# Kernel tuning notes

Hardware: AMD Instinct MI355X
Metric: run time of the kernel (lower is better)

Reference implementation:

```python
import jax, jax.numpy as jnp
import numpy as np

B, S, D, H = 4, 2048, 2048, 16
DH = D // H


def setup_inputs() -> dict:
    key = jax.random.key(0)
    ks = jax.random.split(key, 11)
    p = 0.02  # keep pre-softmax logits in a sane range
    return {
        "x": jax.random.normal(ks[0], (B, S, D), jnp.float32),
        "Wq": jax.random.normal(ks[1], (D, D), jnp.float32) * p,
        "bq": jax.random.normal(ks[2], (D,), jnp.float32) * p,
        "Wk": jax.random.normal(ks[3], (D, D), jnp.float32) * p,
        "bk": jax.random.normal(ks[4], (D,), jnp.float32) * p,
        "Wv": jax.random.normal(ks[5], (D, D), jnp.float32) * p,
        "bv": jax.random.normal(ks[6], (D,), jnp.float32) * p,
        "Wo": jax.random.normal(ks[7], (D, D), jnp.float32) * p,
        "bo": jax.random.normal(ks[8], (D,), jnp.float32) * p,
        "spiral_weight": jax.random.normal(ks[9], (H,), jnp.float32),
        "helix_rotation": jax.random.normal(ks[10], (D,), jnp.float32),
    }


def reference(x, Wq, bq, Wk, bk, Wv, bv, Wo, bo, spiral_weight, helix_rotation):
    b, s, d = x.shape
    h, dh = H, d // H
    # projections (torch Linear: x @ W.T + b), split into heads
    q = (x @ Wq.T + bq).reshape(b, s, h, dh)
    k = (x @ Wk.T + bk).reshape(b, s, h, dh)
    v = (x @ Wv.T + bv).reshape(b, s, h, dh)
    # cos/sin helix gating, applied per (head, head_dim) channel
    rot = helix_rotation.reshape(h, dh)
    q = q * jnp.cos(rot)
    k = k * jnp.sin(rot)
    # per-head scaled scores: [b,h,s,s]
    scores = jnp.einsum("bshd,bthd->bhst", q, k) / np.sqrt(dh).astype(np.float32)
    scores = scores * spiral_weight[None, :, None, None]
    attn = jax.nn.softmax(scores, axis=-1)
    out = jnp.einsum("bhst,bthd->bshd", attn, v).reshape(b, s, d)
    return out @ Wo.T + bo
```

## Files before the change

kernel.cpp:

```cpp
#include <hip/hip_runtime.h>
#include <math.h>

#define B_ 4
#define S_ 2048
#define D_ 2048
#define H_ 16
#define DH_ 128

typedef unsigned short u16;
typedef unsigned int u32;
typedef u16 u16x8 __attribute__((ext_vector_type(8)));
typedef __bf16 bf16x8 __attribute__((ext_vector_type(8)));
typedef float f32x4 __attribute__((ext_vector_type(4)));

__device__ inline u16 f2bf(float f) {
    unsigned int u = __builtin_bit_cast(unsigned int, f);
    unsigned int lsb = (u >> 16) & 1u;
    u += 0x7fffu + lsb;
    return (u16)(u >> 16);
}

__device__ inline f32x4 mfma16(u16x8 a, u16x8 b, f32x4 c) {
    return __builtin_amdgcn_mfma_f32_16x16x32_bf16(
        __builtin_bit_cast(bf16x8, a), __builtin_bit_cast(bf16x8, b), c, 0, 0, 0);
}

__device__ inline void gl2lds16(const u16* g, u16* l) {
    __builtin_amdgcn_global_load_lds(
        (const __attribute__((address_space(1))) void*)g,
        (__attribute__((address_space(3))) void*)l, 16, 0, 0);
}

__global__ __launch_bounds__(256) void cvt_f32_bf16(const float* __restrict__ src,
                                                    u16* __restrict__ dst, int n8) {
    int i = blockIdx.x * 256 + threadIdx.x;
    if (i >= n8) return;
    const float4* s = (const float4*)src + (size_t)i * 2;
    float4 a = s[0], b = s[1];
    u16x8 o;
    o[0] = f2bf(a.x); o[1] = f2bf(a.y); o[2] = f2bf(a.z); o[3] = f2bf(a.w);
    o[4] = f2bf(b.x); o[5] = f2bf(b.y); o[6] = f2bf(b.z); o[7] = f2bf(b.w);
    *((u16x8*)dst + i) = o;
}

template <int GATE, int TRANSV, typename OutT>
__global__ __launch_bounds__(256) void gemm_bt(const u16* __restrict__ A,
                                               const u16* __restrict__ Bw,
                                               const float* __restrict__ bias,
                                               const float* __restrict__ helix,
                                               OutT* __restrict__ C,
                                               int M, int N, int K) {
    __shared__ __align__(16) u16 As[128 * 64];
    __shared__ __align__(16) u16 Bs[128 * 64];

    const int tid = threadIdx.x;
    const int lane = tid & 63, w = tid >> 6;
    const int lr = lane & 15, quad = lane >> 4;
    const int wm = w & 1, wn = w >> 1;
    const int tm = blockIdx.y, tn = blockIdx.x;

    const u16* Ab = A + (size_t)(tm * 128) * K;
    const u16* Bb = Bw + (size_t)(tn * 128) * K;

    const u16* gA[4];
    const u16* gB[4];
    u16* lA[4];
    u16* lB[4];
#pragma unroll
    for (int q = 0; q < 4; ++q) {
        int seg = w * 4 + q;
        int row = seg * 8 + (lane >> 3);
        int gcol = ((lane & 7) ^ (row & 7)) * 8;
        gA[q] = Ab + (size_t)row * K + gcol;
        gB[q] = Bb + (size_t)row * K + gcol;
        lA[q] = As + seg * 512;
        lB[q] = Bs + seg * 512;
    }

    f32x4 zero = {0.f, 0.f, 0.f, 0.f};
    f32x4 acc[4][4];
#pragma unroll
    for (int im = 0; im < 4; ++im)
#pragma unroll
        for (int jn = 0; jn < 4; ++jn) acc[im][jn] = zero;

    const int rA = wm * 64 + lr;
    const int rB = wn * 64 + lr;
    const int sw = lr & 7;

    for (int kt = 0; kt < K; kt += 64) {
        __syncthreads();
#pragma unroll
        for (int q = 0; q < 4; ++q) gl2lds16(gA[q] + kt, lA[q]);
#pragma unroll
        for (int q = 0; q < 4; ++q) gl2lds16(gB[q] + kt, lB[q]);
        __syncthreads();

#pragma unroll
        for (int s = 0; s < 2; ++s) {
            const int kc = ((s * 4 + quad) ^ sw) * 8;
            u16x8 af[4], bf[4];
#pragma unroll
            for (int im = 0; im < 4; ++im)
                af[im] = *(const u16x8*)&As[(rA + im * 16) * 64 + kc];
#pragma unroll
            for (int jn = 0; jn < 4; ++jn)
                bf[jn] = *(const u16x8*)&Bs[(rB + jn * 16) * 64 + kc];
#pragma unroll
            for (int im = 0; im < 4; ++im)
#pragma unroll
                for (int jn = 0; jn < 4; ++jn)
                    acc[im][jn] = mfma16(af[im], bf[jn], acc[im][jn]);
        }
    }

    if constexpr (TRANSV) {
        __shared__ __align__(16) u16 Ts[128 * 72];
        const int grow = tm * 128;
        const int bb = grow / S_;
        const int t0g = grow % S_;
#pragma unroll
        for (int hb = 0; hb < 2; ++hb) {
            __syncthreads();
            if (wm == hb) {
#pragma unroll
                for (int jn = 0; jn < 4; ++jn) {
                    float bs = bias[tn * 128 + wn * 64 + jn * 16 + lr];
#pragma unroll
                    for (int im = 0; im < 4; ++im)
#pragma unroll
                        for (int r = 0; r < 4; ++r)
                            Ts[(wn * 64 + jn * 16 + lr) * 72 + im * 16 + quad * 4 + r] =
                                f2bf(acc[im][jn][r] + bs);
                }
            }
            __syncthreads();
#pragma unroll
            for (int p = 0; p < 4; ++p) {
                int idx = p * 256 + tid;
                int dh_l = idx & 127, tb8 = idx >> 7;
                u16x8 o = *(const u16x8*)&Ts[dh_l * 72 + tb8 * 8];
                int gd = tn * 128 + dh_l;
                int hh = gd >> 7, dhm = gd & 127;
                u16* dst = (u16*)C + (((size_t)bb * H_ + hh) * DH_ + dhm) * S_ + t0g +
                           hb * 64 + tb8 * 8;
                *(u16x8*)dst = o;
            }
        }
    } else {
#pragma unroll
        for (int jn = 0; jn < 4; ++jn) {
            int col = tn * 128 + wn * 64 + jn * 16 + lr;
            float bs = bias[col];
            float g = 1.0f;
            if (GATE == 1) g = cosf(helix[col]);
            if (GATE == 2) g = sinf(helix[col]);
#pragma unroll
            for (int im = 0; im < 4; ++im)
#pragma unroll
                for (int r = 0; r < 4; ++r) {
                    int row = tm * 128 + wm * 64 + im * 16 + quad * 4 + r;
                    float val = (acc[im][jn][r] + bs) * g;
                    if constexpr (sizeof(OutT) == 2)
                        ((u16*)C)[(size_t)row * N + col] = f2bf(val);
                    else
                        ((float*)C)[(size_t)row * N + col] = val;
                }
        }
    }
}

__global__ __launch_bounds__(256, 2) void helix_attn(const u16* __restrict__ Q,
                                                     const u16* __restrict__ Kq,
                                                     const u16* __restrict__ Vt,
                                                     const float* __restrict__ spiral,
                                                     u16* __restrict__ O) {
    __shared__ __align__(16) u16 Ks[64 * 136];
    __shared__ __align__(16) u16 Vs[128 * 72];
    __shared__ __align__(16) u16 Ps[128 * 80];

    const int tid = threadIdx.x;
    const int lane = tid & 63, w = tid >> 6;
    const int lr = lane & 15, quad = lane >> 4;

    const int bx = blockIdx.x;
    const int qt = bx & 15;
    const int h = (bx >> 4) & 15;
    const int b = bx >> 8;

    const size_t headoff = (size_t)b * S_ * D_ + (size_t)h * DH_;
    const u16* qp = Q + headoff;
    const u16* kp = Kq + headoff;
    const u16* vtp = Vt + ((size_t)b * H_ + h) * (size_t)DH_ * S_;

    const float scale2 = spiral[h] * 0.08838834764831845f * 1.4426950408889634f;

    u16x8 qf[2][4];
#pragma unroll
    for (int mb = 0; mb < 2; ++mb)
#pragma unroll
        for (int c = 0; c < 4; ++c) {
            u16x8 raw = *(const u16x8*)(qp + (size_t)(qt * 128 + mb * 64 + w * 16 + lr) * D_ +
                                        c * 32 + quad * 8);
#pragma unroll
            for (int j = 0; j < 8; ++j) {
                float f = __builtin_bit_cast(float, (u32)raw[j] << 16) * scale2;
                qf[mb][c][j] = f2bf(f);
            }
        }

    f32x4 zero = {0.f, 0.f, 0.f, 0.f};
    f32x4 Oacc[2][8];
#pragma unroll
    for (int mb = 0; mb < 2; ++mb)
#pragma unroll
        for (int n = 0; n < 8; ++n) Oacc[mb][n] = zero;
    float rs[2][4] = {{0.f, 0.f, 0.f, 0.f}, {0.f, 0.f, 0.f, 0.f}};

    for (int tt = 0; tt < 32; ++tt) {
        const int t0 = tt * 64;
        __syncthreads();
#pragma unroll
        for (int p = 0; p < 4; ++p) {
            int lin = p * 256 + tid;
            int trow = lin >> 4;
            int ch = (lin & 15) * 8;
            *(u16x8*)&Ks[trow * 136 + ch] =
                *(const u16x8*)(kp + (size_t)(t0 + trow) * D_ + ch);
            int drow = lin >> 3;
            int tch = (lin & 7) * 8;
            *(u16x8*)&Vs[drow * 72 + tch] =
                *(const u16x8*)(vtp + (size_t)drow * S_ + t0 + tch);
        }
        __syncthreads();

        f32x4 Sacc[2][4] = {{zero, zero, zero, zero}, {zero, zero, zero, zero}};
#pragma unroll
        for (int c = 0; c < 4; ++c) {
#pragma unroll
            for (int j = 0; j < 4; ++j) {
                u16x8 kf = *(const u16x8*)&Ks[(j * 16 + lr) * 136 + c * 32 + quad * 8];
                Sacc[0][j] = mfma16(qf[0][c], kf, Sacc[0][j]);
                Sacc[1][j] = mfma16(qf[1][c], kf, Sacc[1][j]);
            }
        }

#pragma unroll
        for (int mb = 0; mb < 2; ++mb)
#pragma unroll
            for (int j = 0; j < 4; ++j)
#pragma unroll
                for (int r = 0; r < 4; ++r) {
                    float p = exp2f(Sacc[mb][j][r]);
                    u32 u = __builtin_bit_cast(u32, p);
                    rs[mb][r] += __builtin_bit_cast(float, u & 0xffff0000u);
                    Ps[(mb * 64 + w * 16 + quad * 4 + r) * 80 + j * 16 + lr] = (u16)(u >> 16);
                }

#pragma unroll
        for (int ks = 0; ks < 2; ++ks) {
            u16x8 pf0 = *(const u16x8*)&Ps[(w * 16 + lr) * 80 + ks * 32 + quad * 8];
            u16x8 pf1 = *(const u16x8*)&Ps[(64 + w * 16 + lr) * 80 + ks * 32 + quad * 8];
#pragma unroll
            for (int n = 0; n < 8; ++n) {
                u16x8 vf = *(const u16x8*)&Vs[(n * 16 + lr) * 72 + ks * 32 + quad * 8];
                Oacc[0][n] = mfma16(pf0, vf, Oacc[0][n]);
                Oacc[1][n] = mfma16(pf1, vf, Oacc[1][n]);
            }
        }
    }

#pragma unroll
    for (int mb = 0; mb < 2; ++mb)
#pragma unroll
        for (int r = 0; r < 4; ++r) {
            float s = rs[mb][r];
#pragma unroll
            for (int off = 1; off < 16; off <<= 1) s += __shfl_xor(s, off, 64);
            float inv = 1.0f / s;
            int row = qt * 128 + mb * 64 + w * 16 + quad * 4 + r;
            u16* op = O + headoff + (size_t)row * D_;
#pragma unroll
            for (int n = 0; n < 8; ++n) op[n * 16 + lr] = f2bf(Oacc[mb][n][r] * inv);
        }
}

extern "C" void kernel_launch(void* const* d_in, const int* in_sizes, int n_in,
                              void* d_out, int out_size, void* d_ws, size_t ws_size,
                              hipStream_t stream) {
    const float* x = (const float*)d_in[0];
    const float* Wq = (const float*)d_in[1];
    const float* bq = (const float*)d_in[2];
    const float* Wk = (const float*)d_in[3];
    const float* bk = (const float*)d_in[4];
    const float* Wv = (const float*)d_in[5];
    const float* bv = (const float*)d_in[6];
    const float* Wo = (const float*)d_in[7];
    const float* bo = (const float*)d_in[8];
    const float* spiral = (const float*)d_in[9];
    const float* helix = (const float*)d_in[10];
    float* out = (float*)d_out;

    char* ws = (char*)d_ws;
    u16* xbf = (u16*)(ws);
    u16* wqb = (u16*)(ws + 33554432);
    u16* wkb = (u16*)(ws + 33554432 + 8388608);
    u16* wvb = (u16*)(ws + 33554432 + 16777216);
    u16* wob = (u16*)(ws + 33554432 + 25165824);
    u16* qb = (u16*)(ws + 67108864);
    u16* kb = (u16*)(ws + 67108864 + 33554432);
    u16* vtb = (u16*)(ws + 67108864 + 67108864);
    u16* attnb = xbf;

    const int ND = D_ * D_;
    const int NX = B_ * S_ * D_;

    cvt_f32_bf16<<<NX / 8 / 256, 256, 0, stream>>>(x, xbf, NX / 8);
    cvt_f32_bf16<<<ND / 8 / 256, 256, 0, stream>>>(Wq, wqb, ND / 8);
    cvt_f32_bf16<<<ND / 8 / 256, 256, 0, stream>>>(Wk, wkb, ND / 8);
    cvt_f32_bf16<<<ND / 8 / 256, 256, 0, stream>>>(Wv, wvb, ND / 8);
    cvt_f32_bf16<<<ND / 8 / 256, 256, 0, stream>>>(Wo, wob, ND / 8);

    dim3 gg(D_ / 128, (B_ * S_) / 128);
    gemm_bt<1, 0, u16><<<gg, 256, 0, stream>>>(xbf, wqb, bq, helix, qb, B_ * S_, D_, D_);
    gemm_bt<2, 0, u16><<<gg, 256, 0, stream>>>(xbf, wkb, bk, helix, kb, B_ * S_, D_, D_);
    gemm_bt<0, 1, u16><<<gg, 256, 0, stream>>>(xbf, wvb, bv, nullptr, vtb, B_ * S_, D_, D_);

    helix_attn<<<B_ * H_ * (S_ / 128), 256, 0, stream>>>(qb, kb, vtb, spiral, attnb);

    gemm_bt<0, 0, float><<<gg, 256, 0, stream>>>(attnb, wob, bo, nullptr, out, B_ * S_, D_, D_);
}
```

Measured before the change: 697.4 us.

## Replace projection GEMMs with 256x256 double-buffered, ping-pong scheduled kernel

Replaces the 128x128 single-buffered GEMM with a 256x256-tile, 512-thread kernel. It double-buffers LDS and splits each k-step into four MFMA quarter phases, issuing the next tile's global-to-LDS loads between them and raising wave priority during MFMA bursts. The V projection is recomputed as Wv·xᵀ, so the output comes out already transposed per head without the LDS transpose epilogue. This aims to hide load latency and raise arithmetic intensity. The costs are a larger LDS footprint (128KB per block), more barriers, and scalar strided stores in the V epilogue.

```diff
diff --git a/kernel.cpp b/kernel.cpp
--- a/kernel.cpp
+++ b/kernel.cpp
@@ -29,6 +29,12 @@
     __builtin_amdgcn_global_load_lds(
         (const __attribute__((address_space(1))) void*)g,
         (__attribute__((address_space(3))) void*)l, 16, 0, 0);
+}
+
+__device__ inline void block_barrier() {
+    asm volatile("" ::: "memory");
+    __builtin_amdgcn_s_barrier();
+    asm volatile("" ::: "memory");
 }
 
 __global__ __launch_bounds__(256) void cvt_f32_bf16(const float* __restrict__ src,
@@ -43,123 +49,188 @@
     *((u16x8*)dst + i) = o;
 }
 
-template <int GATE, int TRANSV, typename OutT>
-__global__ __launch_bounds__(256) void gemm_bt(const u16* __restrict__ A,
-                                               const u16* __restrict__ Bw,
-                                               const float* __restrict__ bias,
-                                               const float* __restrict__ helix,
-                                               OutT* __restrict__ C,
-                                               int M, int N, int K) {
-    __shared__ __align__(16) u16 As[128 * 64];
-    __shared__ __align__(16) u16 Bs[128 * 64];
+template <int GATE, int VOUT, typename OutT>
+__global__ __launch_bounds__(512, 2) void gemm256(const u16* __restrict__ A,
+                                                  const u16* __restrict__ Bw,
+                                                  const float* __restrict__ bias,
+                                                  const float* __restrict__ helix,
+                                                  OutT* __restrict__ C,
+                                                  int M, int N, int K) {
+    __shared__ __align__(16) u16 As[2][256 * 64];
+    __shared__ __align__(16) u16 Bs[2][256 * 64];
 
     const int tid = threadIdx.x;
     const int lane = tid & 63, w = tid >> 6;
     const int lr = lane & 15, quad = lane >> 4;
     const int wm = w & 1, wn = w >> 1;
     const int tm = blockIdx.y, tn = blockIdx.x;
-
-    const u16* Ab = A + (size_t)(tm * 128) * K;
-    const u16* Bb = Bw + (size_t)(tn * 128) * K;
-
-    const u16* gA[4];
-    const u16* gB[4];
-    u16* lA[4];
-    u16* lB[4];
-#pragma unroll
-    for (int q = 0; q < 4; ++q) {
-        int seg = w * 4 + q;
-        int row = seg * 8 + (lane >> 3);
-        int gcol = ((lane & 7) ^ (row & 7)) * 8;
-        gA[q] = Ab + (size_t)row * K + gcol;
-        gB[q] = Bb + (size_t)row * K + gcol;
-        lA[q] = As + seg * 512;
-        lB[q] = Bs + seg * 512;
+    const int NT = K >> 6;
+
+    const u16* Asrc = A + (size_t)(tm * 256) * K;
+    const u16* Bsrc = Bw + (size_t)(tn * 256) * K;
+
+    u32 go[4][2];
+    u32 lo[4][2];
+#pragma unroll
+    for (int q = 0; q < 2; ++q) {
+        const int seg = w * 2 + q;
+        const int i0 = seg * 8 + (lane >> 3);
+        const int s0 = seg * 8;
+        int row = (i0 & 63) | ((i0 >> 6) << 7);
+        int rb = (s0 & 63) | ((s0 >> 6) << 7);
+        go[0][q] = (u32)row * K + (((lane & 7) ^ (row & 7)) << 3);
+        lo[0][q] = rb << 6;
+        row += 64; rb += 64;
+        go[3][q] = (u32)row * K + (((lane & 7) ^ (row & 7)) << 3);
+        lo[3][q] = rb << 6;
+        row = (i0 & 31) | ((i0 >> 5) << 6);
+        rb = (s0 & 31) | ((s0 >> 5) << 6);
+        go[1][q] = (u32)row * K + (((lane & 7) ^ (row & 7)) << 3);
+        lo[1][q] = rb << 6;
+        row += 32; rb += 32;
+        go[2][q] = (u32)row * K + (((lane & 7) ^ (row & 7)) << 3);
+        lo[2][q] = rb << 6;
     }
 
+#define STAGE(u, tt)                                                          \
+    do {                                                                      \
+        const int kt_ = (((tt) < NT) ? (tt) : (NT - 1)) << 6;                 \
+        const u16* gb_ = ((u) == 1 || (u) == 2) ? Bsrc : Asrc;                \
+        u16* lb_ = ((u) == 1 || (u) == 2) ? Bs[(tt) & 1] : As[(tt) & 1];      \
+        gl2lds16(gb_ + go[u][0] + kt_, lb_ + lo[u][0]);                       \
+        gl2lds16(gb_ + go[u][1] + kt_, lb_ + lo[u][1]);                       \
+    } while (0)
+
+    const int koff0 = (quad * 8) ^ ((lr & 7) * 8);
+    const int koff1 = (32 + quad * 8) ^ ((lr & 7) * 8);
+    const int rA = wm * 128 + lr;
+    const int rB = wn * 64 + lr;
+
     f32x4 zero = {0.f, 0.f, 0.f, 0.f};
-    f32x4 acc[4][4];
-#pragma unroll
-    for (int im = 0; im < 4; ++im)
+    f32x4 acc[8][4];
+#pragma unroll
+    for (int im = 0; im < 8; ++im)
 #pragma unroll
         for (int jn = 0; jn < 4; ++jn) acc[im][jn] = zero;
 
-    const int rA = wm * 64 + lr;
-    const int rB = wn * 64 + lr;
-    const int sw = lr & 7;
-
-    for (int kt = 0; kt < K; kt += 64) {
-        __syncthreads();
-#pragma unroll
-        for (int q = 0; q < 4; ++q) gl2lds16(gA[q] + kt, lA[q]);
-#pragma unroll
-        for (int q = 0; q < 4; ++q) gl2lds16(gB[q] + kt, lB[q]);
-        __syncthreads();
-
-#pragma unroll
-        for (int s = 0; s < 2; ++s) {
-            const int kc = ((s * 4 + quad) ^ sw) * 8;
-            u16x8 af[4], bf[4];
+    u16x8 af[4][2], bf[4][2];
+
+    STAGE(0, 0); STAGE(1, 0); STAGE(2, 0); STAGE(3, 0);
+    STAGE(0, 1); STAGE(1, 1); STAGE(2, 1);
+    asm volatile("s_waitcnt vmcnt(6)" ::: "memory");
+    block_barrier();
+
+    for (int t = 0; t < NT; ++t) {
+        const u16* Ab = As[t & 1];
+        const u16* Bb = Bs[t & 1];
+
+#pragma unroll
+        for (int im = 0; im < 4; ++im) {
+            af[im][0] = *(const u16x8*)&Ab[(rA + im * 16) * 64 + koff0];
+            af[im][1] = *(const u16x8*)&Ab[(rA + im * 16) * 64 + koff1];
+        }
+#pragma unroll
+        for (int jn = 0; jn < 2; ++jn) {
+            bf[jn][0] = *(const u16x8*)&Bb[(rB + jn * 16) * 64 + koff0];
+            bf[jn][1] = *(const u16x8*)&Bb[(rB + jn * 16) * 64 + koff1];
+        }
+        STAGE(3, t + 1);
+        block_barrier();
+        asm volatile("s_waitcnt lgkmcnt(0)" ::: "memory");
+        __builtin_amdgcn_s_setprio(1);
+#pragma unroll
+        for (int s = 0; s < 2; ++s)
 #pragma unroll
             for (int im = 0; im < 4; ++im)
-                af[im] = *(const u16x8*)&As[(rA + im * 16) * 64 + kc];
-#pragma unroll
-            for (int jn = 0; jn < 4; ++jn)
-                bf[jn] = *(const u16x8*)&Bs[(rB + jn * 16) * 64 + kc];
+#pragma unroll
+                for (int jn = 0; jn < 2; ++jn)
+                    acc[im][jn] = mfma16(af[im][s], bf[jn][s], acc[im][jn]);
+        __builtin_amdgcn_s_setprio(0);
+        block_barrier();
+
+#pragma unroll
+        for (int jn = 2; jn < 4; ++jn) {
+            bf[jn][0] = *(const u16x8*)&Bb[(rB + jn * 16) * 64 + koff0];
+            bf[jn][1] = *(const u16x8*)&Bb[(rB + jn * 16) * 64 + koff1];
+        }
+        STAGE(0, t + 2);
+        block_barrier();
+        asm volatile("s_waitcnt lgkmcnt(0)" ::: "memory");
+        __builtin_amdgcn_s_setprio(1);
+#pragma unroll
+        for (int s = 0; s < 2; ++s)
 #pragma unroll
             for (int im = 0; im < 4; ++im)
 #pragma unroll
-                for (int jn = 0; jn < 4; ++jn)
-                    acc[im][jn] = mfma16(af[im], bf[jn], acc[im][jn]);
-        }
+                for (int jn = 2; jn < 4; ++jn)
+                    acc[im][jn] = mfma16(af[im][s], bf[jn][s], acc[im][jn]);
+        __builtin_amdgcn_s_setprio(0);
+        block_barrier();
+
+#pragma unroll
+        for (int im = 0; im < 4; ++im) {
+            af[im][0] = *(const u16x8*)&Ab[(rA + 64 + im * 16) * 64 + koff0];
+            af[im][1] = *(const u16x8*)&Ab[(rA + 64 + im * 16) * 64 + koff1];
+        }
+        STAGE(1, t + 2);
+        block_barrier();
+        asm volatile("s_waitcnt lgkmcnt(0)" ::: "memory");
+        __builtin_amdgcn_s_setprio(1);
+#pragma unroll
+        for (int s = 0; s < 2; ++s)
+#pragma unroll
+            for (int im = 0; im < 4; ++im)
+#pragma unroll
+                for (int jn = 0; jn < 2; ++jn)
+                    acc[im + 4][jn] = mfma16(af[im][s], bf[jn][s], acc[im + 4][jn]);
+        __builtin_amdgcn_s_setprio(0);
+        block_barrier();
+
+        STAGE(2, t + 2);
+        asm volatile("s_waitcnt vmcnt(6)" ::: "memory");
+        block_barrier();
+        __builtin_amdgcn_s_setprio(1);
+#pragma unroll
+        for (int s = 0; s < 2; ++s)
+#pragma unroll
+            for (int im = 0; im < 4; ++im)
+#pragma unroll
+                for (int jn = 2; jn < 4; ++jn)
+                    acc[im + 4][jn] = mfma16(af[im][s], bf[jn][s], acc[im + 4][jn]);
+        __builtin_amdgcn_s_setprio(0);
+        block_barrier();
     }
-
-    if constexpr (TRANSV) {
-        __shared__ __align__(16) u16 Ts[128 * 72];
-        const int grow = tm * 128;
-        const int bb = grow / S_;
-        const int t0g = grow % S_;
-#pragma unroll
-        for (int hb = 0; hb < 2; ++hb) {
-            __syncthreads();
-            if (wm == hb) {
+    asm volatile("s_waitcnt vmcnt(0)" ::: "memory");
+#undef STAGE
+
+    if constexpr (VOUT) {
+#pragma unroll
+        for (int im = 0; im < 8; ++im)
+#pragma unroll
+            for (int r = 0; r < 4; ++r) {
+                int row = tm * 256 + wm * 128 + im * 16 + quad * 4 + r;
+                float bs = bias[row];
 #pragma unroll
                 for (int jn = 0; jn < 4; ++jn) {
-                    float bs = bias[tn * 128 + wn * 64 + jn * 16 + lr];
-#pragma unroll
-                    for (int im = 0; im < 4; ++im)
-#pragma unroll
-                        for (int r = 0; r < 4; ++r)
-                            Ts[(wn * 64 + jn * 16 + lr) * 72 + im * 16 + quad * 4 + r] =
-                                f2bf(acc[im][jn][r] + bs);
+                    int col = tn * 256 + wn * 64 + jn * 16 + lr;
+                    float val = acc[im][jn][r] + bs;
+                    ((u16*)C)[(size_t)(col >> 11) * ((size_t)D_ * S_) +
+                              (size_t)row * S_ + (col & (S_ - 1))] = f2bf(val);
                 }
             }
-            __syncthreads();
-#pragma unroll
-            for (int p = 0; p < 4; ++p) {
-                int idx = p * 256 + tid;
-                int dh_l = idx & 127, tb8 = idx >> 7;
-                u16x8 o = *(const u16x8*)&Ts[dh_l * 72 + tb8 * 8];
-                int gd = tn * 128 + dh_l;
-                int hh = gd >> 7, dhm = gd & 127;
-                u16* dst = (u16*)C + (((size_t)bb * H_ + hh) * DH_ + dhm) * S_ + t0g +
-                           hb * 64 + tb8 * 8;
-                *(u16x8*)dst = o;
-            }
-        }
     } else {
 #pragma unroll
         for (int jn = 0; jn < 4; ++jn) {
-            int col = tn * 128 + wn * 64 + jn * 16 + lr;
+            int col = tn * 256 + wn * 64 + jn * 16 + lr;
             float bs = bias[col];
             float g = 1.0f;
             if (GATE == 1) g = cosf(helix[col]);
             if (GATE == 2) g = sinf(helix[col]);
 #pragma unroll
-            for (int im = 0; im < 4; ++im)
+            for (int im = 0; im < 8; ++im)
 #pragma unroll
                 for (int r = 0; r < 4; ++r) {
-                    int row = tm * 128 + wm * 64 + im * 16 + quad * 4 + r;
+                    int row = tm * 256 + wm * 128 + im * 16 + quad * 4 + r;
                     float val = (acc[im][jn][r] + bs) * g;
                     if constexpr (sizeof(OutT) == 2)
                         ((u16*)C)[(size_t)row * N + col] = f2bf(val);
@@ -321,12 +392,13 @@
     cvt_f32_bf16<<<ND / 8 / 256, 256, 0, stream>>>(Wv, wvb, ND / 8);
     cvt_f32_bf16<<<ND / 8 / 256, 256, 0, stream>>>(Wo, wob, ND / 8);
 
-    dim3 gg(D_ / 128, (B_ * S_) / 128);
-    gemm_bt<1, 0, u16><<<gg, 256, 0, stream>>>(xbf, wqb, bq, helix, qb, B_ * S_, D_, D_);
-    gemm_bt<2, 0, u16><<<gg, 256, 0, stream>>>(xbf, wkb, bk, helix, kb, B_ * S_, D_, D_);
-    gemm_bt<0, 1, u16><<<gg, 256, 0, stream>>>(xbf, wvb, bv, nullptr, vtb, B_ * S_, D_, D_);
+    dim3 gq(D_ / 256, (B_ * S_) / 256);
+    gemm256<1, 0, u16><<<gq, 512, 0, stream>>>(xbf, wqb, bq, helix, qb, B_ * S_, D_, D_);
+    gemm256<2, 0, u16><<<gq, 512, 0, stream>>>(xbf, wkb, bk, helix, kb, B_ * S_, D_, D_);
+    dim3 gv((B_ * S_) / 256, D_ / 256);
+    gemm256<0, 1, u16><<<gv, 512, 0, stream>>>(wvb, xbf, bv, nullptr, vtb, D_, B_ * S_, D_);
 
     helix_attn<<<B_ * H_ * (S_ / 128), 256, 0, stream>>>(qb, kb, vtb, spiral, attnb);
 
-    gemm_bt<0, 0, float><<<gg, 256, 0, stream>>>(attnb, wob, bo, nullptr, out, B_ * S_, D_, D_);
-}
+    gemm256<0, 0, float><<<gq, 512, 0, stream>>>(attnb, wob, bo, nullptr, out, B_ * S_, D_, D_);
+}
```

Result: no change. 703.2 us (+0.8%).
